# Performance work log

Measured on AMD Instinct MI355X. Metric: run time of the kernel, lower is better.

Reference implementation:

```python
import jax, jax.numpy as jnp
import numpy as np

SEQ_LEN = 1024
CHANNELS = 64
UNITS = 32
WIDTH = 64
BATCH = 4
EPS = 1e-7


def setup_inputs() -> dict:
    key = jax.random.key(0)
    ks = jax.random.split(key, 5)
    x = jax.random.normal(ks[0], (BATCH, CHANNELS, SEQ_LEN), dtype=jnp.float32)
    Wt = jax.random.normal(ks[1], (UNITS, CHANNELS), dtype=jnp.float32) * (1.0 / np.sqrt(CHANNELS))
    Wx = jax.random.normal(ks[2], (UNITS, CHANNELS), dtype=jnp.float32) * (1.0 / np.sqrt(CHANNELS))
    Wa_w = jax.random.normal(ks[3], (1, UNITS), dtype=jnp.float32) * (1.0 / np.sqrt(UNITS))
    Wa_b = jnp.zeros((1,), dtype=jnp.float32)
    bh = jnp.zeros((UNITS,), dtype=jnp.float32)
    return {"x": x, "Wt": Wt, "Wx": Wx, "Wa_w": Wa_w, "Wa_b": Wa_b, "bh": bh}


def reference(x, Wt, Wx, Wa_w, Wa_b, bh):
    # x: (B, C, S) -> xt: (B, S, C)
    xt = jnp.transpose(x, (0, 2, 1))
    q = jnp.einsum('bsc,uc->bsu', xt, Wt)          # (B, S, U)
    k = jnp.einsum('bsc,uc->bsu', xt, Wx)          # (B, S, U)
    # additive (Bahdanau) scores: tanh over broadcast sum -> (B, S, S, U)
    h = jnp.tanh(q[:, :, None, :] + k[:, None, :, :] + bh)
    e = jnp.einsum('bstu,u->bst', h, Wa_w[0]) + Wa_b[0]   # (B, S, S)
    e = jnp.exp(e - jnp.max(e, axis=-1, keepdims=True))
    # local window mask: key index t allowed for query s iff s-W//2 <= t < s-W//2+W
    idx = jnp.arange(SEQ_LEN)
    lower = idx - WIDTH // 2                        # (S,)
    mask = (lower[:, None] <= idx[None, :]) & (idx[None, :] < (lower[:, None] + WIDTH))
    e = e * mask.astype(e.dtype)
    a = e / (jnp.sum(e, axis=-1, keepdims=True) + EPS)    # (B, S, S)
    v = jnp.einsum('bst,btc->bsc', a, xt)           # (B, S, C)
    v = jnp.transpose(v, (0, 2, 1))                 # (B, C, S)
    return (v, a)
```

## Files before the change

kernel.cpp:

```cpp
#include <hip/hip_runtime.h>
#include <cstddef>
#include <cmath>

#define SEQ    1024
#define CH     64
#define UNITS  32
#define WIDTH  64
#define HALFW  32
#define BATCH  4
#define EPS    1e-7f

#define TS     8
#define TT     80
#define XTS    68
#define KTS    36
#define SCS    68
#define VTS    68

__global__ __launch_bounds__(256) void qk_kernel(
    const float* __restrict__ x, const float* __restrict__ Wt,
    const float* __restrict__ Wx, const float* __restrict__ bh,
    float* __restrict__ q, float* __restrict__ k)
{
    int bu = blockIdx.x;
    int u  = bu & (UNITS - 1);
    int b  = bu >> 5;
    int s4 = (int)threadIdx.x << 2;

    const float* wt = Wt + u * CH;
    const float* wx = Wx + u * CH;
    const float* xb = x + (size_t)b * CH * SEQ + s4;

    float4 qa = {0.f, 0.f, 0.f, 0.f};
    float4 ka = {0.f, 0.f, 0.f, 0.f};
#pragma unroll
    for (int c = 0; c < CH; ++c) {
        float4 xv = *reinterpret_cast<const float4*>(xb + (size_t)c * SEQ);
        float wtc = wt[c], wxc = wx[c];
        qa.x = fmaf(xv.x, wtc, qa.x); qa.y = fmaf(xv.y, wtc, qa.y);
        qa.z = fmaf(xv.z, wtc, qa.z); qa.w = fmaf(xv.w, wtc, qa.w);
        ka.x = fmaf(xv.x, wxc, ka.x); ka.y = fmaf(xv.y, wxc, ka.y);
        ka.z = fmaf(xv.z, wxc, ka.z); ka.w = fmaf(xv.w, wxc, ka.w);
    }
    float bv = bh[u];
    qa.x += bv; qa.y += bv; qa.z += bv; qa.w += bv;
    size_t o = (size_t)bu * SEQ + s4;
    *reinterpret_cast<float4*>(q + o) = qa;
    *reinterpret_cast<float4*>(k + o) = ka;
}

__global__ __launch_bounds__(256) void attn_kernel(
    const float* __restrict__ x,
    const float* __restrict__ qp, const float* __restrict__ k,
    const float* __restrict__ Wa_w, const float* __restrict__ Wa_b,
    float* __restrict__ out)
{
    __shared__ __align__(16) float xT[TT * XTS];
    __shared__ __align__(16) float kT[TT * KTS];
    __shared__ __align__(16) float qT[TS * KTS];
    __shared__ __align__(16) float sc[TS * SCS];
    __shared__ __align__(16) float vt[TS * VTS];
    __shared__ __align__(16) float wa_s[UNITS];
    __shared__ float wab_s;

    int tid = threadIdx.x;
    int blk = blockIdx.x;
    int b   = blk >> 7;
    int s0  = (blk & 127) << 3;
    int t0  = s0 - HALFW;

    const float* xb = x  + (size_t)b * CH * SEQ;
    const float* qb = qp + (size_t)b * UNITS * SEQ;
    const float* kb = k  + (size_t)b * UNITS * SEQ;

#pragma unroll
    for (int i = 0; i < 5; ++i) {
        int idx = i * 256 + tid;
        int cg = idx / TT;
        int tt = idx - cg * TT;
        int t = t0 + tt; t = t < 0 ? 0 : (t > SEQ - 1 ? SEQ - 1 : t);
        float4 v4;
        v4.x = xb[(4 * cg + 0) * SEQ + t];
        v4.y = xb[(4 * cg + 1) * SEQ + t];
        v4.z = xb[(4 * cg + 2) * SEQ + t];
        v4.w = xb[(4 * cg + 3) * SEQ + t];
        *reinterpret_cast<float4*>(&xT[tt * XTS + 4 * cg]) = v4;
    }
#pragma unroll
    for (int i = 0; i < 3; ++i) {
        int idx = i * 256 + tid;
        if (idx < TT * (UNITS / 4)) {
            int uq = idx / TT;
            int tt = idx - uq * TT;
            int t = t0 + tt; t = t < 0 ? 0 : (t > SEQ - 1 ? SEQ - 1 : t);
            float4 v4;
            v4.x = kb[(4 * uq + 0) * SEQ + t];
            v4.y = kb[(4 * uq + 1) * SEQ + t];
            v4.z = kb[(4 * uq + 2) * SEQ + t];
            v4.w = kb[(4 * uq + 3) * SEQ + t];
            *reinterpret_cast<float4*>(&kT[tt * KTS + 4 * uq]) = v4;
        }
    }
    if (tid < 64) {
        int sl = tid >> 3, uq = tid & 7;
        float4 v4;
        v4.x = qb[(4 * uq + 0) * SEQ + s0 + sl];
        v4.y = qb[(4 * uq + 1) * SEQ + s0 + sl];
        v4.z = qb[(4 * uq + 2) * SEQ + s0 + sl];
        v4.w = qb[(4 * uq + 3) * SEQ + s0 + sl];
        *reinterpret_cast<float4*>(&qT[sl * KTS + 4 * uq]) = v4;
    }
    if (tid < UNITS) wa_s[tid] = Wa_w[tid];
    if (tid == 0)    wab_s = Wa_b[0];
    __syncthreads();

    if (tid < 128) {
        int sl = tid >> 4, tq = tid & 15;
        int j0 = 4 * tq;
        float e0 = wab_s, e1 = wab_s, e2 = wab_s, e3 = wab_s;
#pragma unroll
        for (int uq = 0; uq < 8; ++uq) {
            float4 q4 = *reinterpret_cast<const float4*>(&qT[sl * KTS + 4 * uq]);
            float4 w4 = *reinterpret_cast<const float4*>(&wa_s[4 * uq]);
#pragma unroll
            for (int e = 0; e < 4; ++e) {
                float4 k4 = *reinterpret_cast<const float4*>(
                    &kT[(sl + j0 + e) * KTS + 4 * uq]);
                float z0 = q4.x + k4.x, z1 = q4.y + k4.y;
                float z2 = q4.z + k4.z, z3 = q4.w + k4.w;
                float t0f = 1.f - 2.f * __builtin_amdgcn_rcpf(__expf(2.f * z0) + 1.f);
                float t1f = 1.f - 2.f * __builtin_amdgcn_rcpf(__expf(2.f * z1) + 1.f);
                float t2f = 1.f - 2.f * __builtin_amdgcn_rcpf(__expf(2.f * z2) + 1.f);
                float t3f = 1.f - 2.f * __builtin_amdgcn_rcpf(__expf(2.f * z3) + 1.f);
                float acc = fmaf(t0f, w4.x, fmaf(t1f, w4.y,
                            fmaf(t2f, w4.z, t3f * w4.w)));
                if      (e == 0) e0 += acc;
                else if (e == 1) e1 += acc;
                else if (e == 2) e2 += acc;
                else             e3 += acc;
            }
        }
        int tb = t0 + sl + j0;
        if (tb + 0 < 0 || tb + 0 >= SEQ) e0 = -INFINITY;
        if (tb + 1 < 0 || tb + 1 >= SEQ) e1 = -INFINITY;
        if (tb + 2 < 0 || tb + 2 >= SEQ) e2 = -INFINITY;
        if (tb + 3 < 0 || tb + 3 >= SEQ) e3 = -INFINITY;

        float m = fmaxf(fmaxf(e0, e1), fmaxf(e2, e3));
#pragma unroll
        for (int off = 8; off >= 1; off >>= 1) m = fmaxf(m, __shfl_xor(m, off));
        float p0 = __expf(e0 - m), p1 = __expf(e1 - m);
        float p2 = __expf(e2 - m), p3 = __expf(e3 - m);
        float ssum = (p0 + p1) + (p2 + p3);
#pragma unroll
        for (int off = 8; off >= 1; off >>= 1) ssum += __shfl_xor(ssum, off);
        float inv = __builtin_amdgcn_rcpf(ssum + EPS);
        float4 a4 = {p0 * inv, p1 * inv, p2 * inv, p3 * inv};
        *reinterpret_cast<float4*>(&sc[sl * SCS + j0]) = a4;
    }
    __syncthreads();

    int jh  = tid >> 7;
    int r   = tid & 127;
    int slv = r >> 4;
    int cg  = r & 15;
    float4 acc = {0.f, 0.f, 0.f, 0.f};
#pragma unroll 8
    for (int jj = 0; jj < 32; ++jj) {
        int j = jh * 32 + jj;
        float a = sc[slv * SCS + j];
        float4 x4 = *reinterpret_cast<const float4*>(
            &xT[(slv + j) * XTS + 4 * cg]);
        acc.x = fmaf(a, x4.x, acc.x);
        acc.y = fmaf(a, x4.y, acc.y);
        acc.z = fmaf(a, x4.z, acc.z);
        acc.w = fmaf(a, x4.w, acc.w);
    }
    if (jh == 1)
        *reinterpret_cast<float4*>(&vt[slv * VTS + 4 * cg]) = acc;
    __syncthreads();

    if (jh == 0) {
        float4 p = *reinterpret_cast<const float4*>(&vt[slv * VTS + 4 * cg]);
        acc.x += p.x; acc.y += p.y; acc.z += p.z; acc.w += p.w;
        *reinterpret_cast<float4*>(&vt[slv * VTS + 4 * cg]) = acc;
    } else {
        float* abase = out + (size_t)BATCH * CH * SEQ
                           + ((size_t)(b * SEQ + s0)) * SEQ;
#pragma unroll
        for (int i = 0; i < 16; ++i) {
            int slot = i * 128 + r;
            int row  = slot >> 8;
            int i0   = (slot & 255) << 2;
            int d = i0 - (s0 + row - HALFW);
            float4 w4 = {0.f, 0.f, 0.f, 0.f};
            if (d > -4 && d < WIDTH) {
                const float* srow = &sc[row * SCS];
                if (d >= 0     && d     < WIDTH) w4.x = srow[d];
                if (d + 1 >= 0 && d + 1 < WIDTH) w4.y = srow[d + 1];
                if (d + 2 >= 0 && d + 2 < WIDTH) w4.z = srow[d + 2];
                if (d + 3 >= 0 && d + 3 < WIDTH) w4.w = srow[d + 3];
            }
            *reinterpret_cast<float4*>(&abase[(size_t)row * SEQ + i0]) = w4;
        }
    }
    __syncthreads();

    float* vbase = out + ((size_t)b * CH) * SEQ + s0;
#pragma unroll
    for (int i = 0; i < 2; ++i) {
        int idx = i * 256 + tid;
        int c = idx >> 3, sl2 = idx & 7;
        vbase[(size_t)c * SEQ + sl2] = vt[sl2 * VTS + c];
    }
}

extern "C" void kernel_launch(void* const* d_in, const int* in_sizes, int n_in,
                              void* d_out, int out_size, void* d_ws, size_t ws_size,
                              hipStream_t stream) {
    const float* x    = (const float*)d_in[0];
    const float* Wt   = (const float*)d_in[1];
    const float* Wx   = (const float*)d_in[2];
    const float* Wa_w = (const float*)d_in[3];
    const float* Wa_b = (const float*)d_in[4];
    const float* bh   = (const float*)d_in[5];
    float* out = (float*)d_out;

    float* q  = (float*)d_ws;
    float* kk = q + (size_t)BATCH * UNITS * SEQ;

    qk_kernel<<<BATCH * UNITS, 256, 0, stream>>>(x, Wt, Wx, bh, q, kk);
    attn_kernel<<<BATCH * (SEQ / TS), 256, 0, stream>>>(x, q, kk, Wa_w, Wa_b, out);
}
```

Before: 83.69 us.

## Double query tile per attention block and restructure score, AV, and output stages

Each attention block now handles 16 query rows instead of 8, so all 256 threads compute scores and the staged x/k window is reused across more rows. The split-j AV reduction through shared memory and its extra barriers are removed: each thread computes a full 64-term dot product and writes v directly to global memory. The qk kernel is split into two half-sequence blocks of 128 threads to raise block count. Trade-offs are half as many attention blocks, which lowers parallelism, and strided, less coalesced v stores.

```diff
diff --git a/kernel.cpp b/kernel.cpp
--- a/kernel.cpp
+++ b/kernel.cpp
@@ -10,22 +10,22 @@
 #define BATCH  4
 #define EPS    1e-7f
 
-#define TS     8
+#define TS     16
 #define TT     80
 #define XTS    68
 #define KTS    36
 #define SCS    68
-#define VTS    68
-
-__global__ __launch_bounds__(256) void qk_kernel(
+
+__global__ __launch_bounds__(128) void qk_kernel(
     const float* __restrict__ x, const float* __restrict__ Wt,
     const float* __restrict__ Wx, const float* __restrict__ bh,
     float* __restrict__ q, float* __restrict__ k)
 {
-    int bu = blockIdx.x;
-    int u  = bu & (UNITS - 1);
-    int b  = bu >> 5;
-    int s4 = (int)threadIdx.x << 2;
+    int blk = blockIdx.x;
+    int b  = blk >> 6;
+    int u  = (blk >> 1) & (UNITS - 1);
+    int h  = blk & 1;
+    int s4 = h * (SEQ / 2) + (int)threadIdx.x * 4;
 
     const float* wt = Wt + u * CH;
     const float* wx = Wx + u * CH;
@@ -44,7 +44,7 @@
     }
     float bv = bh[u];
     qa.x += bv; qa.y += bv; qa.z += bv; qa.w += bv;
-    size_t o = (size_t)bu * SEQ + s4;
+    size_t o = ((size_t)(b * UNITS + u)) * SEQ + s4;
     *reinterpret_cast<float4*>(q + o) = qa;
     *reinterpret_cast<float4*>(k + o) = ka;
 }
@@ -59,14 +59,13 @@
     __shared__ __align__(16) float kT[TT * KTS];
     __shared__ __align__(16) float qT[TS * KTS];
     __shared__ __align__(16) float sc[TS * SCS];
-    __shared__ __align__(16) float vt[TS * VTS];
     __shared__ __align__(16) float wa_s[UNITS];
     __shared__ float wab_s;
 
     int tid = threadIdx.x;
     int blk = blockIdx.x;
-    int b   = blk >> 7;
-    int s0  = (blk & 127) << 3;
+    int b   = blk >> 6;
+    int s0  = (blk & 63) << 4;
     int t0  = s0 - HALFW;
 
     const float* xb = x  + (size_t)b * CH * SEQ;
@@ -101,117 +100,99 @@
             *reinterpret_cast<float4*>(&kT[tt * KTS + 4 * uq]) = v4;
         }
     }
-    if (tid < 64) {
-        int sl = tid >> 3, uq = tid & 7;
+    if (tid < 128) {
+        int r = tid >> 3, uq = tid & 7;
         float4 v4;
-        v4.x = qb[(4 * uq + 0) * SEQ + s0 + sl];
-        v4.y = qb[(4 * uq + 1) * SEQ + s0 + sl];
-        v4.z = qb[(4 * uq + 2) * SEQ + s0 + sl];
-        v4.w = qb[(4 * uq + 3) * SEQ + s0 + sl];
-        *reinterpret_cast<float4*>(&qT[sl * KTS + 4 * uq]) = v4;
+        v4.x = qb[(4 * uq + 0) * SEQ + s0 + r];
+        v4.y = qb[(4 * uq + 1) * SEQ + s0 + r];
+        v4.z = qb[(4 * uq + 2) * SEQ + s0 + r];
+        v4.w = qb[(4 * uq + 3) * SEQ + s0 + r];
+        *reinterpret_cast<float4*>(&qT[r * KTS + 4 * uq]) = v4;
     }
     if (tid < UNITS) wa_s[tid] = Wa_w[tid];
     if (tid == 0)    wab_s = Wa_b[0];
     __syncthreads();
 
-    if (tid < 128) {
-        int sl = tid >> 4, tq = tid & 15;
-        int j0 = 4 * tq;
-        float e0 = wab_s, e1 = wab_s, e2 = wab_s, e3 = wab_s;
+    {
+        int r = tid >> 4, tq = tid & 15;
+        float ev[4] = {wab_s, wab_s, wab_s, wab_s};
 #pragma unroll
         for (int uq = 0; uq < 8; ++uq) {
-            float4 q4 = *reinterpret_cast<const float4*>(&qT[sl * KTS + 4 * uq]);
+            float4 q4 = *reinterpret_cast<const float4*>(&qT[r * KTS + 4 * uq]);
             float4 w4 = *reinterpret_cast<const float4*>(&wa_s[4 * uq]);
 #pragma unroll
             for (int e = 0; e < 4; ++e) {
                 float4 k4 = *reinterpret_cast<const float4*>(
-                    &kT[(sl + j0 + e) * KTS + 4 * uq]);
+                    &kT[(r + tq + 16 * e) * KTS + 4 * uq]);
                 float z0 = q4.x + k4.x, z1 = q4.y + k4.y;
                 float z2 = q4.z + k4.z, z3 = q4.w + k4.w;
-                float t0f = 1.f - 2.f * __builtin_amdgcn_rcpf(__expf(2.f * z0) + 1.f);
-                float t1f = 1.f - 2.f * __builtin_amdgcn_rcpf(__expf(2.f * z1) + 1.f);
-                float t2f = 1.f - 2.f * __builtin_amdgcn_rcpf(__expf(2.f * z2) + 1.f);
-                float t3f = 1.f - 2.f * __builtin_amdgcn_rcpf(__expf(2.f * z3) + 1.f);
-                float acc = fmaf(t0f, w4.x, fmaf(t1f, w4.y,
-                            fmaf(t2f, w4.z, t3f * w4.w)));
-                if      (e == 0) e0 += acc;
-                else if (e == 1) e1 += acc;
-                else if (e == 2) e2 += acc;
-                else             e3 += acc;
+                float a0 = 1.f - 2.f * __builtin_amdgcn_rcpf(__expf(2.f * z0) + 1.f);
+                float a1 = 1.f - 2.f * __builtin_amdgcn_rcpf(__expf(2.f * z1) + 1.f);
+                float a2 = 1.f - 2.f * __builtin_amdgcn_rcpf(__expf(2.f * z2) + 1.f);
+                float a3 = 1.f - 2.f * __builtin_amdgcn_rcpf(__expf(2.f * z3) + 1.f);
+                ev[e] += fmaf(a0, w4.x, fmaf(a1, w4.y,
+                         fmaf(a2, w4.z, a3 * w4.w)));
             }
         }
-        int tb = t0 + sl + j0;
-        if (tb + 0 < 0 || tb + 0 >= SEQ) e0 = -INFINITY;
-        if (tb + 1 < 0 || tb + 1 >= SEQ) e1 = -INFINITY;
-        if (tb + 2 < 0 || tb + 2 >= SEQ) e2 = -INFINITY;
-        if (tb + 3 < 0 || tb + 3 >= SEQ) e3 = -INFINITY;
-
-        float m = fmaxf(fmaxf(e0, e1), fmaxf(e2, e3));
+#pragma unroll
+        for (int e = 0; e < 4; ++e) {
+            int t = t0 + r + tq + 16 * e;
+            if (t < 0 || t >= SEQ) ev[e] = -INFINITY;
+        }
+        float m = fmaxf(fmaxf(ev[0], ev[1]), fmaxf(ev[2], ev[3]));
 #pragma unroll
         for (int off = 8; off >= 1; off >>= 1) m = fmaxf(m, __shfl_xor(m, off));
-        float p0 = __expf(e0 - m), p1 = __expf(e1 - m);
-        float p2 = __expf(e2 - m), p3 = __expf(e3 - m);
+        float p0 = __expf(ev[0] - m), p1 = __expf(ev[1] - m);
+        float p2 = __expf(ev[2] - m), p3 = __expf(ev[3] - m);
         float ssum = (p0 + p1) + (p2 + p3);
 #pragma unroll
         for (int off = 8; off >= 1; off >>= 1) ssum += __shfl_xor(ssum, off);
         float inv = __builtin_amdgcn_rcpf(ssum + EPS);
-        float4 a4 = {p0 * inv, p1 * inv, p2 * inv, p3 * inv};
-        *reinterpret_cast<float4*>(&sc[sl * SCS + j0]) = a4;
+        sc[r * SCS + tq]      = p0 * inv;
+        sc[r * SCS + tq + 16] = p1 * inv;
+        sc[r * SCS + tq + 32] = p2 * inv;
+        sc[r * SCS + tq + 48] = p3 * inv;
     }
     __syncthreads();
 
-    int jh  = tid >> 7;
-    int r   = tid & 127;
-    int slv = r >> 4;
-    int cg  = r & 15;
-    float4 acc = {0.f, 0.f, 0.f, 0.f};
-#pragma unroll 8
-    for (int jj = 0; jj < 32; ++jj) {
-        int j = jh * 32 + jj;
-        float a = sc[slv * SCS + j];
-        float4 x4 = *reinterpret_cast<const float4*>(
-            &xT[(slv + j) * XTS + 4 * cg]);
-        acc.x = fmaf(a, x4.x, acc.x);
-        acc.y = fmaf(a, x4.y, acc.y);
-        acc.z = fmaf(a, x4.z, acc.z);
-        acc.w = fmaf(a, x4.w, acc.w);
-    }
-    if (jh == 1)
-        *reinterpret_cast<float4*>(&vt[slv * VTS + 4 * cg]) = acc;
-    __syncthreads();
-
-    if (jh == 0) {
-        float4 p = *reinterpret_cast<const float4*>(&vt[slv * VTS + 4 * cg]);
-        acc.x += p.x; acc.y += p.y; acc.z += p.z; acc.w += p.w;
-        *reinterpret_cast<float4*>(&vt[slv * VTS + 4 * cg]) = acc;
-    } else {
-        float* abase = out + (size_t)BATCH * CH * SEQ
-                           + ((size_t)(b * SEQ + s0)) * SEQ;
-#pragma unroll
-        for (int i = 0; i < 16; ++i) {
-            int slot = i * 128 + r;
-            int row  = slot >> 8;
-            int i0   = (slot & 255) << 2;
-            int d = i0 - (s0 + row - HALFW);
-            float4 w4 = {0.f, 0.f, 0.f, 0.f};
-            if (d > -4 && d < WIDTH) {
-                const float* srow = &sc[row * SCS];
-                if (d >= 0     && d     < WIDTH) w4.x = srow[d];
-                if (d + 1 >= 0 && d + 1 < WIDTH) w4.y = srow[d + 1];
-                if (d + 2 >= 0 && d + 2 < WIDTH) w4.z = srow[d + 2];
-                if (d + 3 >= 0 && d + 3 < WIDTH) w4.w = srow[d + 3];
-            }
-            *reinterpret_cast<float4*>(&abase[(size_t)row * SEQ + i0]) = w4;
-        }
-    }
-    __syncthreads();
-
-    float* vbase = out + ((size_t)b * CH) * SEQ + s0;
-#pragma unroll
-    for (int i = 0; i < 2; ++i) {
-        int idx = i * 256 + tid;
-        int c = idx >> 3, sl2 = idx & 7;
-        vbase[(size_t)c * SEQ + sl2] = vt[sl2 * VTS + c];
+    float* abase = out + (size_t)BATCH * CH * SEQ
+                       + ((size_t)(b * SEQ + s0)) * SEQ;
+#pragma unroll
+    for (int i = 0; i < 16; ++i) {
+        int slot = i * 256 + tid;
+        int row  = slot >> 8;
+        int i0   = (slot & 255) << 2;
+        int d = i0 - (s0 + row - HALFW);
+        float4 w4 = {0.f, 0.f, 0.f, 0.f};
+        if (d > -4 && d < WIDTH) {
+            const float* srow = &sc[row * SCS];
+            if (d >= 0     && d     < WIDTH) w4.x = srow[d];
+            if (d + 1 >= 0 && d + 1 < WIDTH) w4.y = srow[d + 1];
+            if (d + 2 >= 0 && d + 2 < WIDTH) w4.z = srow[d + 2];
+            if (d + 3 >= 0 && d + 3 < WIDTH) w4.w = srow[d + 3];
+        }
+        *reinterpret_cast<float4*>(&abase[(size_t)row * SEQ + i0]) = w4;
+    }
+
+    {
+        int sl = tid & 15, cg = tid >> 4;
+        float4 acc = {0.f, 0.f, 0.f, 0.f};
+        const float* arow = &sc[sl * SCS];
+#pragma unroll 16
+        for (int j = 0; j < WIDTH; ++j) {
+            float a = arow[j];
+            float4 x4 = *reinterpret_cast<const float4*>(
+                &xT[(sl + j) * XTS + 4 * cg]);
+            acc.x = fmaf(a, x4.x, acc.x);
+            acc.y = fmaf(a, x4.y, acc.y);
+            acc.z = fmaf(a, x4.z, acc.z);
+            acc.w = fmaf(a, x4.w, acc.w);
+        }
+        float* vb = out + ((size_t)b * CH + 4 * cg) * SEQ + s0 + sl;
+        vb[0 * SEQ] = acc.x;
+        vb[1 * SEQ] = acc.y;
+        vb[2 * SEQ] = acc.z;
+        vb[3 * SEQ] = acc.w;
     }
 }
 
@@ -229,6 +210,6 @@
     float* q  = (float*)d_ws;
     float* kk = q + (size_t)BATCH * UNITS * SEQ;
 
-    qk_kernel<<<BATCH * UNITS, 256, 0, stream>>>(x, Wt, Wx, bh, q, kk);
+    qk_kernel<<<BATCH * UNITS * 2, 128, 0, stream>>>(x, Wt, Wx, bh, q, kk);
     attn_kernel<<<BATCH * (SEQ / TS), 256, 0, stream>>>(x, q, kk, Wa_w, Wa_b, out);
 }
```

Result: faster. 79.81 us (-4.6%).
